# Performance work log

Measured on AMD Instinct MI355X. Metric: run time of the kernel, lower is better.

## Reference

```python
import jax, jax.numpy as jnp
import numpy as np

B = 16384
D = 1024          # entity_dim
N_LAYERS = 4
TEMPERATURE = 32.0  # sqrt(entity_dim)


def setup_inputs() -> dict:
    key = jax.random.key(0)
    ks = jax.random.split(key, 6)
    d2 = 2 * D
    scale = 1.0 / np.sqrt(d2)
    x1 = jax.random.normal(ks[0], (B, D), dtype=jnp.float32)
    x2 = jax.random.normal(ks[1], (B, D), dtype=jnp.float32)
    # stacked per-layer Linear(2D, 2D) params; torch Linear stores W as [out, in]
    Ws = jax.random.normal(ks[2], (N_LAYERS, d2, d2), dtype=jnp.float32) * scale
    bs = jax.random.normal(ks[3], (N_LAYERS, d2), dtype=jnp.float32) * scale
    W_last = jax.random.normal(ks[4], (D, d2), dtype=jnp.float32) * scale
    b_last = jax.random.normal(ks[5], (D,), dtype=jnp.float32) * scale
    return {"x1": x1, "x2": x2, "Ws": Ws, "bs": bs, "W_last": W_last, "b_last": b_last}


def reference(x1, x2, Ws, bs, W_last, b_last):
    # x: [B, 2, D]
    x = jnp.stack((x1, x2), axis=1)
    # attn: [B, 2, 2] -- tiny self-attention over the 2 tokens
    attn = jnp.einsum('bsd,btd->bst', x / TEMPERATURE, x)
    attn = jax.nn.softmax(attn, axis=-1)  # dropout = identity in eval mode
    x = jnp.einsum('bst,btd->bsd', attn, x)
    # concat the two attended tokens -> [B, 2D]
    h = jnp.concatenate((x[:, 0, :], x[:, 1, :]), axis=-1)
    for i in range(N_LAYERS):
        h = jax.nn.relu(h @ Ws[i].T + bs[i])
    return h @ W_last.T + b_last
```

## Files before the change

kernel.cpp:

```cpp
#include <hip/hip_runtime.h>

typedef __bf16 bf16x8 __attribute__((ext_vector_type(8)));
typedef float f32x4 __attribute__((ext_vector_type(4)));

__device__ __forceinline__ unsigned short f2bf(float f) {
    unsigned int u = __builtin_bit_cast(unsigned int, f);
    u += 0x7FFFu + ((u >> 16) & 1u);
    return (unsigned short)(u >> 16);
}

__global__ void cvt_kernel(const float* __restrict__ in,
                           unsigned short* __restrict__ out, long n4) {
    long i = (long)blockIdx.x * blockDim.x + threadIdx.x;
    long stride = (long)gridDim.x * blockDim.x;
    for (; i < n4; i += stride) {
        float4 v = ((const float4*)in)[i];
        ushort4 o;
        o.x = f2bf(v.x); o.y = f2bf(v.y); o.z = f2bf(v.z); o.w = f2bf(v.w);
        ((ushort4*)out)[i] = o;
    }
}

__global__ __launch_bounds__(256) void attn_kernel(
    const float* __restrict__ x1, const float* __restrict__ x2,
    unsigned short* __restrict__ h) {
    const int D = 1024;
    const int lane = threadIdx.x & 63;
    const int wave = threadIdx.x >> 6;
    const long row = (long)blockIdx.x * 4 + wave;
    const float4* p1 = (const float4*)(x1 + row * D);
    const float4* p2 = (const float4*)(x2 + row * D);
    float4 v1[4], v2[4];
    float s11 = 0.f, s12 = 0.f, s22 = 0.f;
#pragma unroll
    for (int j = 0; j < 4; ++j) {
        v1[j] = p1[lane + 64 * j];
        v2[j] = p2[lane + 64 * j];
        s11 += v1[j].x * v1[j].x + v1[j].y * v1[j].y + v1[j].z * v1[j].z + v1[j].w * v1[j].w;
        s12 += v1[j].x * v2[j].x + v1[j].y * v2[j].y + v1[j].z * v2[j].z + v1[j].w * v2[j].w;
        s22 += v2[j].x * v2[j].x + v2[j].y * v2[j].y + v2[j].z * v2[j].z + v2[j].w * v2[j].w;
    }
#pragma unroll
    for (int off = 1; off < 64; off <<= 1) {
        s11 += __shfl_xor(s11, off);
        s12 += __shfl_xor(s12, off);
        s22 += __shfl_xor(s22, off);
    }
    const float a00 = 1.f / (1.f + expf((s12 - s11) * (1.f / 32.f)));
    const float a10 = 1.f / (1.f + expf((s22 - s12) * (1.f / 32.f)));
    const float a01 = 1.f - a00, a11 = 1.f - a10;
    unsigned short* h0 = h + row * 2048;
#pragma unroll
    for (int j = 0; j < 4; ++j) {
        const int f = lane + 64 * j;
        ushort4 o0, o1;
        o0.x = f2bf(a00 * v1[j].x + a01 * v2[j].x);
        o0.y = f2bf(a00 * v1[j].y + a01 * v2[j].y);
        o0.z = f2bf(a00 * v1[j].z + a01 * v2[j].z);
        o0.w = f2bf(a00 * v1[j].w + a01 * v2[j].w);
        o1.x = f2bf(a10 * v1[j].x + a11 * v2[j].x);
        o1.y = f2bf(a10 * v1[j].y + a11 * v2[j].y);
        o1.z = f2bf(a10 * v1[j].z + a11 * v2[j].z);
        o1.w = f2bf(a10 * v1[j].w + a11 * v2[j].w);
        ((ushort4*)(h0))[f] = o0;
        ((ushort4*)(h0 + 1024))[f] = o1;
    }
}

#define BAR   __builtin_amdgcn_s_barrier()
#define LGKM0 asm volatile("s_waitcnt lgkmcnt(0)" ::: "memory")
#define VMW(n) asm volatile("s_waitcnt vmcnt(" #n ")" ::: "memory")
#define PRIO1 __builtin_amdgcn_s_setprio(1)
#define PRIO0 __builtin_amdgcn_s_setprio(0)

#define MMQ(mb, kk)                                                            \
  _Pragma("unroll") for (int n = 0; n < 4; ++n)                                \
  _Pragma("unroll") for (int mq = 0; mq < 4; ++mq)                             \
    acc[(mb) + mq][n] = __builtin_amdgcn_mfma_f32_16x16x32_bf16(               \
        Bf[n][kk], Af[mq][kk], acc[(mb) + mq][n], 0, 0, 0);

template <bool RELU, typename OT>
__global__ __launch_bounds__(512, 2) void gemm256(
    const unsigned short* __restrict__ A,
    const unsigned short* __restrict__ Bw,
    const float* __restrict__ bias,
    OT* __restrict__ C,
    int N, int K) {
    __shared__ __align__(16) unsigned short lds[65536];
    const int tid = threadIdx.x;
    const int lane = tid & 63, wave = tid >> 6;
    const int wm = wave >> 2, wn = wave & 3;
    const int fr = lane & 15, fq = lane >> 4;

    const int cpx = (int)gridDim.x >> 3;
    const int swz = ((int)blockIdx.x & 7) * cpx + ((int)blockIdx.x >> 3);
    const int bm = swz & 63;
    const int bn = swz >> 6;
    const long m0 = (long)bm * 256, n0 = (long)bn * 256;

    const int x0 = fq ^ (fr & 7);
    const int lane_base = fr * 128 + x0 * 16;
    const int aBase = wm * 16384 + lane_base;
    const int bBase = 32768 + (wn >> 1) * 16384 + (wn & 1) * 8192 + lane_base;
    const char* ldsc = (const char*)lds;

    const int l3 = lane >> 3, l7 = lane & 7;
    const long rowb = (long)K * 2;
    const long lane_src = (long)l3 * rowb + ((l7 ^ l3) << 4);
    const char* Abl = (const char*)A + m0 * rowb + lane_src;
    const char* Bbl = (const char*)Bw + n0 * rowb + lane_src;

    auto stage = [&](const char* mb, int matOff, int hf, int kt, int T) {
#pragma unroll
        for (int r = 0; r < 2; ++r) {
            const int W = r * 8 + wave;
            const char* src = mb + (long)(hf * 128 + W * 8) * rowb + kt * 128;
            __builtin_amdgcn_global_load_lds(
                (const __attribute__((address_space(1))) void*)src,
                (__attribute__((address_space(3))) void*)((char*)lds +
                    (T * 65536 + matOff + hf * 16384 + W * 1024)),
                16, 0, 0);
        }
    };

    f32x4 acc[8][4] = {};
    bf16x8 Bf[4][2], Af[4][2];

    auto readBA = [&](int boff, int kk) {
        const int x = kk * 64;
#pragma unroll
        for (int n = 0; n < 4; ++n)
            Bf[n][kk] = *(const bf16x8*)(ldsc + boff + (bBase ^ x) + n * 2048);
#pragma unroll
        for (int m = 0; m < 4; ++m)
            Af[m][kk] = *(const bf16x8*)(ldsc + boff + (aBase ^ x) + m * 2048);
    };
    auto readAH = [&](int boff) {
#pragma unroll
        for (int m = 0; m < 4; ++m) {
            Af[m][0] = *(const bf16x8*)(ldsc + boff + aBase + (m + 4) * 2048);
            Af[m][1] = *(const bf16x8*)(ldsc + boff + (aBase ^ 64) + (m + 4) * 2048);
        }
    };

    stage(Abl, 0,     0, 0, 0); stage(Abl, 0,     1, 0, 0);
    stage(Bbl, 32768, 0, 0, 0); stage(Bbl, 32768, 1, 0, 0);
    stage(Abl, 0,     0, 1, 1); stage(Abl, 0,     1, 1, 1);
    VMW(4);
    BAR;

    const int NT = K >> 6;
    const int NIT = NT >> 1;
    for (int i = 0; i < NIT; ++i) {
        const int t1 = 2 * i + 1, t2 = t1 + 1, t3 = t1 + 2;
        const bool g = (i + 1 < NIT);

        readBA(0, 0);
        stage(Bbl, 32768, 0, t1, 1); stage(Bbl, 32768, 1, t1, 1);
        BAR; PRIO1; MMQ(0, 0); PRIO0; BAR;
        readBA(0, 1);
        BAR; PRIO1; MMQ(0, 1); PRIO0; BAR;
        readAH(0);
        LGKM0;
        BAR; PRIO1; MMQ(4, 0); PRIO0; BAR;
        if (g) { stage(Abl, 0, 0, t2, 0); stage(Abl, 0, 1, t2, 0); }
        BAR; PRIO1; MMQ(4, 1); PRIO0;
        if (g) { VMW(4); } else { VMW(0); }
        BAR;

        readBA(65536, 0);
        if (g) { stage(Bbl, 32768, 0, t2, 0); stage(Bbl, 32768, 1, t2, 0); }
        BAR; PRIO1; MMQ(0, 0); PRIO0; BAR;
        readBA(65536, 1);
        BAR; PRIO1; MMQ(0, 1); PRIO0; BAR;
        readAH(65536);
        LGKM0;
        BAR; PRIO1; MMQ(4, 0); PRIO0; BAR;
        if (g) { stage(Abl, 0, 0, t3, 1); stage(Abl, 0, 1, t3, 1); }
        BAR; PRIO1; MMQ(4, 1); PRIO0;
        if (g) { VMW(4); } else { VMW(0); }
        BAR;
    }

    const long crow0 = m0 + wm * 128 + fr;
    const long ccol0 = n0 + wn * 64 + fq * 4;
    float4 bv[4];
#pragma unroll
    for (int n = 0; n < 4; ++n) bv[n] = *(const float4*)(bias + ccol0 + n * 16);
#pragma unroll
    for (int m = 0; m < 8; ++m) {
        const long rb = (crow0 + m * 16) * N;
#pragma unroll
        for (int n = 0; n < 4; ++n) {
            float v0 = acc[m][n][0] + bv[n].x;
            float v1 = acc[m][n][1] + bv[n].y;
            float v2 = acc[m][n][2] + bv[n].z;
            float v3 = acc[m][n][3] + bv[n].w;
            if (RELU) {
                v0 = v0 > 0.f ? v0 : 0.f; v1 = v1 > 0.f ? v1 : 0.f;
                v2 = v2 > 0.f ? v2 : 0.f; v3 = v3 > 0.f ? v3 : 0.f;
            }
            if constexpr (sizeof(OT) == 2) {
                uint2 o;
                o.x = (unsigned)f2bf(v0) | ((unsigned)f2bf(v1) << 16);
                o.y = (unsigned)f2bf(v2) | ((unsigned)f2bf(v3) << 16);
                *(uint2*)((unsigned short*)C + rb + ccol0 + n * 16) = o;
            } else {
                *(float4*)((float*)C + rb + ccol0 + n * 16) =
                    make_float4(v0, v1, v2, v3);
            }
        }
    }
}

extern "C" void kernel_launch(void* const* d_in, const int* in_sizes, int n_in,
                              void* d_out, int out_size, void* d_ws, size_t ws_size,
                              hipStream_t stream) {
    const float* x1 = (const float*)d_in[0];
    const float* x2 = (const float*)d_in[1];
    const float* Ws = (const float*)d_in[2];
    const float* bs = (const float*)d_in[3];
    const float* Wl = (const float*)d_in[4];
    const float* bl = (const float*)d_in[5];
    float* out = (float*)d_out;

    char* ws = (char*)d_ws;
    unsigned short* hA  = (unsigned short*)(ws);
    unsigned short* hB  = (unsigned short*)(ws + (67108864L));
    unsigned short* Wbf = (unsigned short*)(ws + (134217728L));
    unsigned short* Wlb = (unsigned short*)(ws + (167772160L));

    cvt_kernel<<<2048, 256, 0, stream>>>(Ws, Wbf, 4L * 2048 * 2048 / 4);
    cvt_kernel<<<512, 256, 0, stream>>>(Wl, Wlb, 1024L * 2048 / 4);

    attn_kernel<<<16384 / 4, 256, 0, stream>>>(x1, x2, hA);

    gemm256<true, unsigned short><<<512, 512, 0, stream>>>(hA, Wbf + 0L * 2048 * 2048, bs + 0 * 2048, hB, 2048, 2048);
    gemm256<true, unsigned short><<<512, 512, 0, stream>>>(hB, Wbf + 1L * 2048 * 2048, bs + 1 * 2048, hA, 2048, 2048);
    gemm256<true, unsigned short><<<512, 512, 0, stream>>>(hA, Wbf + 2L * 2048 * 2048, bs + 2 * 2048, hB, 2048, 2048);
    gemm256<true, unsigned short><<<512, 512, 0, stream>>>(hB, Wbf + 3L * 2048 * 2048, bs + 3 * 2048, hA, 2048, 2048);
    gemm256<false, float><<<256, 512, 0, stream>>>(hA, Wlb, bl, out, 1024, 2048);
}
```

Baseline: 662.4 us.

## Software-pipeline LDS fragment reads one MFMA phase ahead with double A registers

Restructures the GEMM main loop so that the LDS reads for the next MFMA quarter are issued before the current quarter's MFMAs, using two ping-pong A register sets (Ap/Aq). The barriers around each MFMA block are reduced to one per phase, and the explicit lgkmcnt waits are removed. The global-to-LDS staging schedule also changes: A and B for the odd tile are both staged during the first half, and a full vmcnt(0) drain replaces the partial waits. The goal is to hide LDS latency behind matrix work and cut barrier overhead. The costs are higher register pressure and a full memory drain twice per iteration, which may expose global load latency.

```diff
diff --git a/kernel.cpp b/kernel.cpp
--- a/kernel.cpp
+++ b/kernel.cpp
@@ -68,16 +68,20 @@
 }
 
 #define BAR   __builtin_amdgcn_s_barrier()
-#define LGKM0 asm volatile("s_waitcnt lgkmcnt(0)" ::: "memory")
-#define VMW(n) asm volatile("s_waitcnt vmcnt(" #n ")" ::: "memory")
+#define VMW0  asm volatile("s_waitcnt vmcnt(0)" ::: "memory")
 #define PRIO1 __builtin_amdgcn_s_setprio(1)
 #define PRIO0 __builtin_amdgcn_s_setprio(0)
 
-#define MMQ(mb, kk)                                                            \
+#define MM03(kk, AR)                                                           \
   _Pragma("unroll") for (int n = 0; n < 4; ++n)                                \
   _Pragma("unroll") for (int mq = 0; mq < 4; ++mq)                             \
-    acc[(mb) + mq][n] = __builtin_amdgcn_mfma_f32_16x16x32_bf16(               \
-        Bf[n][kk], Af[mq][kk], acc[(mb) + mq][n], 0, 0, 0);
+    acc[mq][n] = __builtin_amdgcn_mfma_f32_16x16x32_bf16(                      \
+        Bf[n][kk], AR[mq], acc[mq][n], 0, 0, 0);
+#define MM47(kk, AR)                                                           \
+  _Pragma("unroll") for (int n = 0; n < 4; ++n)                                \
+  _Pragma("unroll") for (int mq = 0; mq < 4; ++mq)                             \
+    acc[4 + mq][n] = __builtin_amdgcn_mfma_f32_16x16x32_bf16(                  \
+        Bf[n][kk], AR[mq], acc[4 + mq][n], 0, 0, 0);
 
 template <bool RELU, typename OT>
 __global__ __launch_bounds__(512, 2) void gemm256(
@@ -124,62 +128,65 @@
     };
 
     f32x4 acc[8][4] = {};
-    bf16x8 Bf[4][2], Af[4][2];
-
-    auto readBA = [&](int boff, int kk) {
-        const int x = kk * 64;
+    bf16x8 Bf[4][2], Ap[4], Aq[4];
+
+    auto rdB = [&](int boff, int kk) {
 #pragma unroll
         for (int n = 0; n < 4; ++n)
-            Bf[n][kk] = *(const bf16x8*)(ldsc + boff + (bBase ^ x) + n * 2048);
+            Bf[n][kk] = *(const bf16x8*)(ldsc + boff + (bBase ^ (kk << 6)) + n * 2048);
+    };
+    auto rdA03 = [&](int boff, int kk, bf16x8 (&D)[4]) {
 #pragma unroll
         for (int m = 0; m < 4; ++m)
-            Af[m][kk] = *(const bf16x8*)(ldsc + boff + (aBase ^ x) + m * 2048);
-    };
-    auto readAH = [&](int boff) {
-#pragma unroll
-        for (int m = 0; m < 4; ++m) {
-            Af[m][0] = *(const bf16x8*)(ldsc + boff + aBase + (m + 4) * 2048);
-            Af[m][1] = *(const bf16x8*)(ldsc + boff + (aBase ^ 64) + (m + 4) * 2048);
-        }
+            D[m] = *(const bf16x8*)(ldsc + boff + (aBase ^ (kk << 6)) + m * 2048);
+    };
+    auto rdA47 = [&](int boff, int kk, bf16x8 (&D)[4]) {
+#pragma unroll
+        for (int m = 0; m < 4; ++m)
+            D[m] = *(const bf16x8*)(ldsc + boff + (aBase ^ (kk << 6)) + (m + 4) * 2048);
     };
 
     stage(Abl, 0,     0, 0, 0); stage(Abl, 0,     1, 0, 0);
     stage(Bbl, 32768, 0, 0, 0); stage(Bbl, 32768, 1, 0, 0);
-    stage(Abl, 0,     0, 1, 1); stage(Abl, 0,     1, 1, 1);
-    VMW(4);
+    VMW0;
     BAR;
+    rdB(0, 0); rdA03(0, 0, Ap);
 
     const int NT = K >> 6;
     const int NIT = NT >> 1;
     for (int i = 0; i < NIT; ++i) {
-        const int t1 = 2 * i + 1, t2 = t1 + 1, t3 = t1 + 2;
+        const int o = 2 * i + 1, e2 = 2 * i + 2;
         const bool g = (i + 1 < NIT);
 
-        readBA(0, 0);
-        stage(Bbl, 32768, 0, t1, 1); stage(Bbl, 32768, 1, t1, 1);
-        BAR; PRIO1; MMQ(0, 0); PRIO0; BAR;
-        readBA(0, 1);
-        BAR; PRIO1; MMQ(0, 1); PRIO0; BAR;
-        readAH(0);
-        LGKM0;
-        BAR; PRIO1; MMQ(4, 0); PRIO0; BAR;
-        if (g) { stage(Abl, 0, 0, t2, 0); stage(Abl, 0, 1, t2, 0); }
-        BAR; PRIO1; MMQ(4, 1); PRIO0;
-        if (g) { VMW(4); } else { VMW(0); }
-        BAR;
-
-        readBA(65536, 0);
-        if (g) { stage(Bbl, 32768, 0, t2, 0); stage(Bbl, 32768, 1, t2, 0); }
-        BAR; PRIO1; MMQ(0, 0); PRIO0; BAR;
-        readBA(65536, 1);
-        BAR; PRIO1; MMQ(0, 1); PRIO0; BAR;
-        readAH(65536);
-        LGKM0;
-        BAR; PRIO1; MMQ(4, 0); PRIO0; BAR;
-        if (g) { stage(Abl, 0, 0, t3, 1); stage(Abl, 0, 1, t3, 1); }
-        BAR; PRIO1; MMQ(4, 1); PRIO0;
-        if (g) { VMW(4); } else { VMW(0); }
-        BAR;
+        rdB(0, 1); rdA03(0, 1, Aq);
+        stage(Abl, 0, 0, o, 1); stage(Abl, 0, 1, o, 1);
+        PRIO1; MM03(0, Ap); PRIO0; BAR;
+
+        rdA47(0, 0, Ap);
+        stage(Bbl, 32768, 0, o, 1); stage(Bbl, 32768, 1, o, 1);
+        PRIO1; MM03(1, Aq); PRIO0; BAR;
+
+        rdA47(0, 1, Aq);
+        PRIO1; MM47(0, Ap); PRIO0; BAR;
+
+        VMW0; BAR;
+        rdB(65536, 0); rdA03(65536, 0, Ap);
+        PRIO1; MM47(1, Aq); PRIO0; BAR;
+
+        rdB(65536, 1); rdA03(65536, 1, Aq);
+        if (g) { stage(Abl, 0, 0, e2, 0); stage(Abl, 0, 1, e2, 0); }
+        PRIO1; MM03(0, Ap); PRIO0; BAR;
+
+        rdA47(65536, 0, Ap);
+        if (g) { stage(Bbl, 32768, 0, e2, 0); stage(Bbl, 32768, 1, e2, 0); }
+        PRIO1; MM03(1, Aq); PRIO0; BAR;
+
+        rdA47(65536, 1, Aq);
+        PRIO1; MM47(0, Ap); PRIO0; BAR;
+
+        VMW0; BAR;
+        if (g) { rdB(0, 0); rdA03(0, 0, Ap); }
+        PRIO1; MM47(1, Aq); PRIO0; BAR;
     }
 
     const long crow0 = m0 + wm * 128 + fr;
@@ -201,10 +208,10 @@
                 v2 = v2 > 0.f ? v2 : 0.f; v3 = v3 > 0.f ? v3 : 0.f;
             }
             if constexpr (sizeof(OT) == 2) {
-                uint2 o;
-                o.x = (unsigned)f2bf(v0) | ((unsigned)f2bf(v1) << 16);
-                o.y = (unsigned)f2bf(v2) | ((unsigned)f2bf(v3) << 16);
-                *(uint2*)((unsigned short*)C + rb + ccol0 + n * 16) = o;
+                uint2 oo;
+                oo.x = (unsigned)f2bf(v0) | ((unsigned)f2bf(v1) << 16);
+                oo.y = (unsigned)f2bf(v2) | ((unsigned)f2bf(v3) << 16);
+                *(uint2*)((unsigned short*)C + rb + ccol0 + n * 16) = oo;
             } else {
                 *(float4*)((float*)C + rb + ccol0 + n * 16) =
                     make_float4(v0, v1, v2, v3);
```

After: 726.8 us. 1.1x slower.
